# Kernel tuning notes

Hardware: AMD Instinct MI355X
Metric: run time of the kernel (lower is better)

## Reference

```python
import jax, jax.numpy as jnp
import numpy as np

B, T, D = 2, 2048, 1024
H, RANK = 16, 32
DH = D // H  # 64


def setup_inputs() -> dict:
    key = jax.random.key(0)
    ks = jax.random.split(key, 6)
    sd = 1.0 / np.sqrt(D)
    sdh = 1.0 / np.sqrt(DH)
    return {
        "x": jax.random.normal(ks[0], (B, T, D), dtype=jnp.float32),
        "W_qkv": jax.random.normal(ks[1], (D, 3 * D), dtype=jnp.float32) * sd,
        "W_q_lsr": jax.random.normal(ks[2], (H, DH, RANK), dtype=jnp.float32) * sdh,
        "W_k_lsr": jax.random.normal(ks[3], (H, DH, RANK), dtype=jnp.float32) * sdh,
        "lsr_core": jnp.ones((H, RANK), dtype=jnp.float32),
        "W_o": jax.random.normal(ks[4], (D, D), dtype=jnp.float32) * sd,
    }


def reference(x, W_qkv, W_q_lsr, W_k_lsr, lsr_core, W_o):
    b, t, d = x.shape
    # Fused QKV projection
    qkv = x @ W_qkv  # (B, T, 3D)
    q, k, v = jnp.split(qkv, 3, axis=-1)
    # (B, H, T, DH)
    q = q.reshape(b, t, H, DH).transpose(0, 2, 1, 3)
    k = k.reshape(b, t, H, DH).transpose(0, 2, 1, 3)
    v = v.reshape(b, t, H, DH).transpose(0, 2, 1, 3)
    # Low-rank bilinear score: q^T Wq diag(core) Wk^T k
    ql = jnp.einsum("bhtd,hdr->bhtr", q, W_q_lsr)  # (B, H, T, R)
    kl = jnp.einsum("bhsd,hdr->bhsr", k, W_k_lsr)  # (B, H, T, R)
    scale = 1.0 / jnp.sqrt(jnp.asarray(RANK, dtype=x.dtype))
    scores = jnp.einsum("bhtr,bhsr->bhts", ql * lsr_core[None, :, None, :], kl) * scale
    # Causal mask
    causal = jnp.tril(jnp.ones((t, t), dtype=bool))
    scores = jnp.where(causal[None, None], scores, jnp.asarray(-jnp.inf, dtype=scores.dtype))
    attn = jax.nn.softmax(scores, axis=-1)
    y = jnp.einsum("bhts,bhsd->bhtd", attn, v)  # (B, H, T, DH)
    y = y.transpose(0, 2, 1, 3).reshape(b, t, d)
    return y @ W_o
```

## Files before the change

### kernel.cpp

```cpp
#include <hip/hip_runtime.h>
#include <hip/hip_bf16.h>

#define B_  2
#define T_  2048
#define D_  1024
#define H_  16
#define DH_ 64
#define R_  32
#define BT_ (B_*T_)
#define BH_ (B_*H_)

typedef unsigned short u16;
typedef unsigned int   u32;
typedef __attribute__((ext_vector_type(8))) short bhalf8;
typedef __attribute__((ext_vector_type(4))) float floatx4;

#define WSB_FLAG  0
#define WSB_XB    256
#define WSB_WCATT (WSB_XB    + 8388608)
#define WSB_QL    (WSB_WCATT + 4194304)
#define WSB_KL    (WSB_QL    + 4194304)
#define WSB_VT    (WSB_KL    + 4194304)
#define WSB_YB    (WSB_VT    + 8388608)
#define WSB_WOT   (WSB_YB    + 8388608)

#define NEG_ -1.0e30f

__device__ __forceinline__ float bfs(u16 s) {
    union { u32 i; float f; } w; w.i = ((u32)s) << 16; return w.f;
}
__device__ __forceinline__ u16 tob(float f) {
    __hip_bfloat16 h = __float2bfloat16(f);
    return *(u16*)&h;
}
__device__ __forceinline__ u32 pack2(float a, float b) {
    return (u32)tob(a) | ((u32)tob(b) << 16);
}
__device__ __forceinline__ void gload16(const u16* g, u16* l) {
    __builtin_amdgcn_global_load_lds(
        (const __attribute__((address_space(1))) void*)g,
        (__attribute__((address_space(3))) void*)l, 16, 0, 0);
}
__device__ __forceinline__ int detect_isbf(const u32* __restrict__ xw, int lane) {
    int hits = 0;
    #pragma unroll
    for (int i = 0; i < 8; ++i) {
        const u32 w = xw[lane + i * 64];
        const u32 h = w & 0xFFFFu;
        const u32 e = (h >> 7) & 0xFFu;
        if (h == 0u || (e >= 100u && e <= 150u)) ++hits;
    }
    #pragma unroll
    for (int off = 32; off; off >>= 1) hits += __shfl_down(hits, off, 64);
    return __shfl(hits, 0, 64) >= 300;
}

__global__ __launch_bounds__(256) void convert_fused(
    const void* __restrict__ x, u16* __restrict__ xb,
    const void* __restrict__ Wqkv, const void* __restrict__ Wo,
    u16* __restrict__ WcatT, u16* __restrict__ WoT)
{
    __shared__ __align__(16) u16 tile[64 * 72];
    const int tid  = threadIdx.x;
    const int lane = tid & 63;
    const int isbf = detect_isbf((const u32*)x, lane);
    const int blk  = blockIdx.x;

    if (blk < 2048) {
        const int e = blk * 256 + tid;
        if (isbf) {
            ((uint4*)xb)[e] = ((const uint4*)x)[e];
        } else {
            float4 a0 = ((const float4*)x)[2*e];
            float4 a1 = ((const float4*)x)[2*e + 1];
            uint4 o;
            o.x = pack2(a0.x, a0.y); o.y = pack2(a0.z, a0.w);
            o.z = pack2(a1.x, a1.y); o.w = pack2(a1.z, a1.w);
            ((uint4*)xb)[e] = o;
        }
        return;
    }

    int t = blk - 2048;
    const void* src; u16* dst; int srcStride, srcColOff, dstRowOff;
    if (t < 256) { src = Wqkv; dst = WcatT; srcStride = 3*D_; srcColOff = 2*D_; dstRowOff = 1024; }
    else { t -= 256; src = Wo; dst = WoT; srcStride = D_; srcColOff = 0; dstRowOff = 0; }
    const int j0 = (t & 15) * 64;
    const int i0 = (t >> 4) * 64;
    #pragma unroll
    for (int p = 0; p < 2; ++p) {
        const int e = tid + p * 256;
        const int r = e >> 3, ch = e & 7;
        if (isbf) {
            uint4 w = *(const uint4*)((const u16*)src + (size_t)(i0 + r) * srcStride + srcColOff + j0 + ch*8);
            *(uint4*)&tile[r * 72 + ch*8] = w;
        } else {
            const float* s = (const float*)src + (size_t)(i0 + r) * srcStride + srcColOff + j0 + ch*8;
            float4 a0 = *(const float4*)s;
            float4 a1 = *(const float4*)(s + 4);
            uint4 o;
            o.x = pack2(a0.x, a0.y); o.y = pack2(a0.z, a0.w);
            o.z = pack2(a1.x, a1.y); o.w = pack2(a1.z, a1.w);
            *(uint4*)&tile[r * 72 + ch*8] = o;
        }
    }
    __syncthreads();
    #pragma unroll
    for (int p = 0; p < 2; ++p) {
        const int e = tid + p * 256;
        const int c = e >> 3, ch = e & 7;
        u16 tmp[8];
        #pragma unroll
        for (int j = 0; j < 8; ++j) tmp[j] = tile[(ch*8 + j) * 72 + c];
        *(uint4*)(dst + (size_t)(dstRowOff + j0 + c) * D_ + i0 + ch*8) = *(uint4*)tmp;
    }
}

__global__ __launch_bounds__(256) void fold_mfma(
    const void* __restrict__ Wqkv, const void* __restrict__ Wq_lsr,
    const void* __restrict__ Wk_lsr, const void* __restrict__ core,
    u16* __restrict__ WcatT, const void* __restrict__ x)
{
    __shared__ __align__(16) u16 Bq[128 * 72];
    __shared__ __align__(16) u16 Bk[128 * 72];
    __shared__ __align__(16) u16 Aq[32 * 72];
    __shared__ __align__(16) u16 Ak[32 * 72];
    const int tid  = threadIdx.x;
    const int lane = tid & 63;
    const int isbf = detect_isbf((const u32*)x, lane);
    const int w    = tid >> 6;
    const int n16  = lane & 15;
    const int q4   = lane >> 4;
    const int h    = blockIdx.y;
    const int d0   = blockIdx.x * 128;

    #pragma unroll
    for (int p = 0; p < 8; ++p) {
        const int e  = tid + p * 256;
        const int r  = e & 31, dh = e >> 5;
        float aq, ak;
        if (isbf) {
            aq = bfs(((const u16*)Wq_lsr)[(h*DH_ + dh)*R_ + r]);
            ak = bfs(((const u16*)Wk_lsr)[(h*DH_ + dh)*R_ + r]);
        } else {
            aq = ((const float*)Wq_lsr)[(h*DH_ + dh)*R_ + r];
            ak = ((const float*)Wk_lsr)[(h*DH_ + dh)*R_ + r];
        }
        Aq[r * 72 + dh] = tob(aq);
        Ak[r * 72 + dh] = tob(ak);
    }
    #pragma unroll
    for (int p = 0; p < 8; ++p) {
        const int e  = tid + p * 256;
        const int n  = e >> 4, ch = e & 15;
        if (isbf) {
            uint2 wq = *(const uint2*)((const u16*)Wqkv + (size_t)(d0+n)*(3*D_) + h*DH_ + ch*4);
            uint2 wk = *(const uint2*)((const u16*)Wqkv + (size_t)(d0+n)*(3*D_) + D_ + h*DH_ + ch*4);
            *(uint2*)&Bq[n * 72 + ch*4] = wq;
            *(uint2*)&Bk[n * 72 + ch*4] = wk;
        } else {
            float4 fq = *(const float4*)((const float*)Wqkv + (size_t)(d0+n)*(3*D_) + h*DH_ + ch*4);
            float4 fk = *(const float4*)((const float*)Wqkv + (size_t)(d0+n)*(3*D_) + D_ + h*DH_ + ch*4);
            uint2 oq, ok;
            oq.x = pack2(fq.x, fq.y); oq.y = pack2(fq.z, fq.w);
            ok.x = pack2(fk.x, fk.y); ok.y = pack2(fk.z, fk.w);
            *(uint2*)&Bq[n * 72 + ch*4] = oq;
            *(uint2*)&Bk[n * 72 + ch*4] = ok;
        }
    }
    __syncthreads();

    floatx4 accq[2][2], acck[2][2];
    #pragma unroll
    for (int mi = 0; mi < 2; ++mi)
        #pragma unroll
        for (int ni = 0; ni < 2; ++ni) { accq[mi][ni] = (floatx4)(0.f); acck[mi][ni] = (floatx4)(0.f); }

    #pragma unroll
    for (int kk = 0; kk < 2; ++kk) {
        bhalf8 aqf[2], akf[2], bqf[2], bkf[2];
        #pragma unroll
        for (int mi = 0; mi < 2; ++mi) {
            aqf[mi] = *(const bhalf8*)&Aq[(mi*16 + n16) * 72 + kk*32 + q4*8];
            akf[mi] = *(const bhalf8*)&Ak[(mi*16 + n16) * 72 + kk*32 + q4*8];
        }
        #pragma unroll
        for (int ni = 0; ni < 2; ++ni) {
            bqf[ni] = *(const bhalf8*)&Bq[(w*32 + ni*16 + n16) * 72 + kk*32 + q4*8];
            bkf[ni] = *(const bhalf8*)&Bk[(w*32 + ni*16 + n16) * 72 + kk*32 + q4*8];
        }
        #pragma unroll
        for (int mi = 0; mi < 2; ++mi)
            #pragma unroll
            for (int ni = 0; ni < 2; ++ni) {
                accq[mi][ni] = __builtin_amdgcn_mfma_f32_16x16x32_bf16(aqf[mi], bqf[ni], accq[mi][ni], 0, 0, 0);
                acck[mi][ni] = __builtin_amdgcn_mfma_f32_16x16x32_bf16(akf[mi], bkf[ni], acck[mi][ni], 0, 0, 0);
            }
    }

    const float scale = (float)(0.17677669529663687 * 1.4426950408889634);
    #pragma unroll
    for (int mi = 0; mi < 2; ++mi) {
        #pragma unroll
        for (int rr = 0; rr < 4; ++rr) {
            const int r = mi*16 + q4*4 + rr;
            const float cc = (isbf ? bfs(((const u16*)core)[h*R_ + r])
                                   : ((const float*)core)[h*R_ + r]) * scale;
            #pragma unroll
            for (int ni = 0; ni < 2; ++ni) {
                const int d = d0 + w*32 + ni*16 + n16;
                WcatT[(size_t)(h*R_ + r) * D_ + d]       = tob(accq[mi][ni][rr] * cc);
                WcatT[(size_t)(512 + h*R_ + r) * D_ + d] = tob(acck[mi][ni][rr]);
            }
        }
    }
}

__global__ __launch_bounds__(256, 4) void gemm1_mfma(
    const u16* __restrict__ xb, const u16* __restrict__ WcatT,
    u16* __restrict__ ql, u16* __restrict__ kl, u16* __restrict__ v_t)
{
    __shared__ __align__(16) u16 As[128 * 64];
    __shared__ __align__(16) u16 Bs[64 * 64];
    const int tid  = threadIdx.x;
    const int lane = tid & 63;
    const int w    = tid >> 6;
    const int n16  = lane & 15;
    const int q4   = lane >> 4;
    const int wx   = w & 1;
    const int wy   = w >> 1;
    const int bm   = blockIdx.y * 128;
    const int bn   = blockIdx.x * 64;
    const int lrow = lane >> 3;
    const int lcol = (lane & 7) * 8;

    floatx4 acc[4][2];
    #pragma unroll
    for (int i = 0; i < 4; ++i)
        #pragma unroll
        for (int j = 0; j < 2; ++j) acc[i][j] = (floatx4)(0.f);

    for (int kt = 0; kt < D_; kt += 64) {
        #pragma unroll
        for (int i = 0; i < 4; ++i) {
            const int r0 = w*32 + i*8;
            gload16(xb + (size_t)(bm + r0 + lrow) * D_ + kt + lcol, &As[r0 * 64]);
        }
        #pragma unroll
        for (int i = 0; i < 2; ++i) {
            const int r0 = w*16 + i*8;
            gload16(WcatT + (size_t)(bn + r0 + lrow) * D_ + kt + lcol, &Bs[r0 * 64]);
        }
        __syncthreads();
        #pragma unroll
        for (int kk = 0; kk < 2; ++kk) {
            bhalf8 a[4], b[2];
            #pragma unroll
            for (int mi = 0; mi < 4; ++mi)
                a[mi] = *(const bhalf8*)&As[(wy*64 + mi*16 + n16) * 64 + kk*32 + q4*8];
            #pragma unroll
            for (int ni = 0; ni < 2; ++ni)
                b[ni] = *(const bhalf8*)&Bs[(wx*32 + ni*16 + n16) * 64 + kk*32 + q4*8];
            #pragma unroll
            for (int mi = 0; mi < 4; ++mi)
                #pragma unroll
                for (int ni = 0; ni < 2; ++ni)
                    acc[mi][ni] = __builtin_amdgcn_mfma_f32_16x16x32_bf16(
                        a[mi], b[ni], acc[mi][ni], 0, 0, 0);
        }
        __syncthreads();
    }

    if (bn < 1024) {
        #pragma unroll
        for (int mi = 0; mi < 4; ++mi) {
            #pragma unroll
            for (int rr = 0; rr < 4; ++rr) {
                const int row = bm + wy*64 + mi*16 + q4*4 + rr;
                const int b   = row >> 11;
                const int t   = row & (T_ - 1);
                #pragma unroll
                for (int ni = 0; ni < 2; ++ni) {
                    const int col = bn + wx*32 + ni*16 + n16;
                    const u16 val = tob(acc[mi][ni][rr]);
                    if (col < 512) {
                        const int h = col >> 5, r = col & 31;
                        ql[((size_t)(b*H_ + h)*T_ + t)*R_ + r] = val;
                    } else {
                        const int c = col - 512; const int h = c >> 5, r = c & 31;
                        kl[((size_t)(b*H_ + h)*T_ + t)*R_ + r] = val;
                    }
                }
            }
        }
    } else {
        #pragma unroll
        for (int mi = 0; mi < 4; ++mi) {
            const int row0 = bm + wy*64 + mi*16 + q4*4;
            const int b = row0 >> 11;
            const int t = row0 & (T_ - 1);
            #pragma unroll
            for (int ni = 0; ni < 2; ++ni) {
                const int c = bn - 1024 + wx*32 + ni*16 + n16;
                const int h = c >> 6, dh = c & 63;
                uint2 o;
                o.x = pack2(acc[mi][ni][0], acc[mi][ni][1]);
                o.y = pack2(acc[mi][ni][2], acc[mi][ni][3]);
                *(uint2*)(v_t + ((size_t)(b*H_ + h) * DH_ + dh) * T_ + t) = o;
            }
        }
    }
}

__device__ __forceinline__ void softmax_update(
    floatx4 (&Sc)[8], float &mrow, float &lrow, floatx4 (&O)[4], int q4)
{
    float cmax[8];
    #pragma unroll
    for (int c = 0; c < 8; ++c)
        cmax[c] = fmaxf(fmaxf(Sc[c][0], Sc[c][1]), fmaxf(Sc[c][2], Sc[c][3]));
    float rmax = fmaxf(fmaxf(fmaxf(cmax[0], cmax[1]), fmaxf(cmax[2], cmax[3])),
                       fmaxf(fmaxf(cmax[4], cmax[5]), fmaxf(cmax[6], cmax[7])));
    rmax = fmaxf(rmax, __shfl_xor(rmax, 16, 64));
    rmax = fmaxf(rmax, __shfl_xor(rmax, 32, 64));

    const float mn = fmaxf(mrow, rmax);
    const int norescale = __all(rmax <= mrow);

    float csum[8];
    #pragma unroll
    for (int c = 0; c < 8; ++c) {
        #pragma unroll
        for (int r = 0; r < 4; ++r)
            Sc[c][r] = __builtin_amdgcn_exp2f(Sc[c][r] - mn);
        csum[c] = (Sc[c][0] + Sc[c][1]) + (Sc[c][2] + Sc[c][3]);
    }
    float rsum = ((csum[0] + csum[1]) + (csum[2] + csum[3]))
               + ((csum[4] + csum[5]) + (csum[6] + csum[7]));
    rsum += __shfl_xor(rsum, 16, 64);
    rsum += __shfl_xor(rsum, 32, 64);

    if (norescale) {
        lrow += rsum;
    } else {
        const float alpha = __builtin_amdgcn_exp2f(mrow - mn);
        mrow = mn;
        lrow = lrow * alpha + rsum;
        float aO[4];
        #pragma unroll
        for (int r = 0; r < 4; ++r) aO[r] = __shfl(alpha, q4*4 + r, 64);
        #pragma unroll
        for (int c2 = 0; c2 < 4; ++c2)
            #pragma unroll
            for (int r = 0; r < 4; ++r) O[c2][r] *= aO[r];
    }
}

__global__ __launch_bounds__(512, 4) void attn_kernel(
    const u16* __restrict__ ql, const u16* __restrict__ kl,
    const u16* __restrict__ v_t, u16* __restrict__ y)
{
    __shared__ __align__(16) u16 kls[128 * 40];
    __shared__ __align__(16) u16 vsT[64 * 136];

    const int tid  = threadIdx.x;
    const int lane = tid & 63;
    const int w    = tid >> 6;
    const int n16  = lane & 15;
    const int q4   = lane >> 4;
    const int bh   = blockIdx.x;
    const int by   = blockIdx.y;
    const int qt2  = (by < 8) ? (15 - by) : (by - 8);
    const int t0   = qt2 * 128;
    const int nt   = qt2 + 1;

    const u16* qlb = ql + (size_t)bh * T_ * R_;
    const bhalf8 aq = *(const bhalf8*)(qlb + (size_t)(t0 + w*16 + n16) * R_ + q4*8);

    const u16* klb = kl  + (size_t)bh * T_ * R_;
    const u16* vtb = v_t + (size_t)bh * DH_ * T_;
    const int rk = tid >> 2, ck = (tid & 3) * 8;
    const int dv = tid >> 4;
    const int m  = tid & 15;
    const int cv = m * 8;
    const int pb = ((m & 1) << 4) | (((m >> 1) & 1) << 2) | ((m >> 2) << 5);

    uint4 kc0 = *(const uint4*)(klb + (size_t)(rk     ) * R_ + ck);
    uint4 vc0 = *(const uint4*)(vtb + (size_t)(dv     ) * T_ + cv);
    uint4 vc1 = *(const uint4*)(vtb + (size_t)(dv + 32) * T_ + cv);
    uint4 kn0 = kc0, vn0 = vc0, vn1 = vc1;

    float mrow = NEG_, lrow = 0.f;
    floatx4 O[4];
    #pragma unroll
    for (int c = 0; c < 4; ++c) O[c] = (floatx4)(0.f);

    for (int it = 0; it < nt; ++it) {
        const int s0 = it * 128;
        __syncthreads();
        *(uint4*)&kls[rk * 40 + ck] = kc0;
        {
            uint2 t;
            t.x = vc0.x; t.y = vc0.y; *(uint2*)&vsT[(dv     ) * 136 + pb    ] = t;
            t.x = vc0.z; t.y = vc0.w; *(uint2*)&vsT[(dv     ) * 136 + pb + 8] = t;
            t.x = vc1.x; t.y = vc1.y; *(uint2*)&vsT[(dv + 32) * 136 + pb    ] = t;
            t.x = vc1.z; t.y = vc1.w; *(uint2*)&vsT[(dv + 32) * 136 + pb + 8] = t;
        }
        if (it + 1 < nt) {
            const int s1 = s0 + 128;
            kn0 = *(const uint4*)(klb + (size_t)(s1 + rk) * R_ + ck);
            vn0 = *(const uint4*)(vtb + (size_t)(dv     ) * T_ + s1 + cv);
            vn1 = *(const uint4*)(vtb + (size_t)(dv + 32) * T_ + s1 + cv);
        }
        __syncthreads();

        floatx4 Sc[8];
        #pragma unroll
        for (int c = 0; c < 8; ++c) {
            bhalf8 ak = *(const bhalf8*)&kls[(16*c + n16) * 40 + q4*8];
            Sc[c] = __builtin_amdgcn_mfma_f32_16x16x32_bf16(ak, aq, (floatx4)(0.f), 0, 0, 0);
        }

        if (it == nt - 1) {
            const int tq = w*16 + n16;
            #pragma unroll
            for (int c = 0; c < 8; ++c) {
                const int sb = 16*c + 4*q4;
                #pragma unroll
                for (int r = 0; r < 4; ++r)
                    if (sb + r > tq) Sc[c][r] = NEG_;
            }
        }

        softmax_update(Sc, mrow, lrow, O, q4);

        #pragma unroll
        for (int kc = 0; kc < 4; ++kc) {
            union { u32 wd[4]; bhalf8 v; } pu;
            pu.wd[0] = pack2(Sc[2*kc    ][0], Sc[2*kc    ][1]);
            pu.wd[1] = pack2(Sc[2*kc    ][2], Sc[2*kc    ][3]);
            pu.wd[2] = pack2(Sc[2*kc + 1][0], Sc[2*kc + 1][1]);
            pu.wd[3] = pack2(Sc[2*kc + 1][2], Sc[2*kc + 1][3]);
            const bhalf8 pa = pu.v;
            #pragma unroll
            for (int c2 = 0; c2 < 4; ++c2) {
                bhalf8 bv = *(const bhalf8*)&vsT[(16*c2 + n16) * 136 + kc*32 + q4*8];
                O[c2] = __builtin_amdgcn_mfma_f32_16x16x32_bf16(pa, bv, O[c2], 0, 0, 0);
            }
        }

        kc0 = kn0; vc0 = vn0; vc1 = vn1;
    }

    const int b = bh >> 4, h = bh & 15;
    float lb[4];
    #pragma unroll
    for (int r = 0; r < 4; ++r) lb[r] = __shfl(lrow, q4*4 + r, 64);
    #pragma unroll
    for (int r = 0; r < 4; ++r) {
        const float rl = 1.0f / lb[r];
        const int t = t0 + w*16 + q4*4 + r;
        #pragma unroll
        for (int c2 = 0; c2 < 4; ++c2)
            y[((size_t)b * T_ + t) * D_ + h * DH_ + 16*c2 + n16] = tob(O[c2][r] * rl);
    }
}

__global__ __launch_bounds__(256, 4) void out_gemm_mfma(
    const u16* __restrict__ yb, const u16* __restrict__ WoT,
    float* __restrict__ out)
{
    __shared__ __align__(16) u16 As[64 * 64];
    __shared__ __align__(16) u16 Bs[64 * 64];
    const int tid  = threadIdx.x;
    const int lane = tid & 63;
    const int w    = tid >> 6;
    const int n16  = lane & 15;
    const int q4   = lane >> 4;
    const int wx   = w & 1;
    const int wy   = w >> 1;
    const int bm   = blockIdx.y * 64;
    const int bn   = blockIdx.x * 64;
    const int lrow = lane >> 3;
    const int lcol = (lane & 7) * 8;

    floatx4 acc[2][2];
    #pragma unroll
    for (int i = 0; i < 2; ++i)
        #pragma unroll
        for (int j = 0; j < 2; ++j) acc[i][j] = (floatx4)(0.f);

    for (int kt = 0; kt < D_; kt += 64) {
        #pragma unroll
        for (int i = 0; i < 2; ++i) {
            const int r0 = w*16 + i*8;
            gload16(yb  + (size_t)(bm + r0 + lrow) * D_ + kt + lcol, &As[r0 * 64]);
            gload16(WoT + (size_t)(bn + r0 + lrow) * D_ + kt + lcol, &Bs[r0 * 64]);
        }
        __syncthreads();
        #pragma unroll
        for (int kk = 0; kk < 2; ++kk) {
            bhalf8 a[2], b[2];
            #pragma unroll
            for (int mi = 0; mi < 2; ++mi)
                a[mi] = *(const bhalf8*)&As[(wy*32 + mi*16 + n16) * 64 + kk*32 + q4*8];
            #pragma unroll
            for (int ni = 0; ni < 2; ++ni)
                b[ni] = *(const bhalf8*)&Bs[(wx*32 + ni*16 + n16) * 64 + kk*32 + q4*8];
            #pragma unroll
            for (int mi = 0; mi < 2; ++mi)
                #pragma unroll
                for (int ni = 0; ni < 2; ++ni)
                    acc[mi][ni] = __builtin_amdgcn_mfma_f32_16x16x32_bf16(
                        a[mi], b[ni], acc[mi][ni], 0, 0, 0);
        }
        __syncthreads();
    }

    #pragma unroll
    for (int mi = 0; mi < 2; ++mi) {
        #pragma unroll
        for (int rr = 0; rr < 4; ++rr) {
            const int row = bm + wy*32 + mi*16 + q4*4 + rr;
            #pragma unroll
            for (int ni = 0; ni < 2; ++ni) {
                const int col = bn + wx*32 + ni*16 + n16;
                out[(size_t)row * D_ + col] = acc[mi][ni][rr];
            }
        }
    }
}

extern "C" void kernel_launch(void* const* d_in, const int* in_sizes, int n_in,
                              void* d_out, int out_size, void* d_ws, size_t ws_size,
                              hipStream_t stream)
{
    (void)out_size; (void)ws_size;
    const void* in_x = nullptr; const void* in_wqkv = nullptr;
    const void* in_wq = nullptr; const void* in_wk = nullptr;
    const void* in_core = nullptr; const void* in_wo = nullptr;
    for (int i = 0; i < n_in; ++i) {
        const int s = in_sizes[i];
        if      (s == BT_*D_)     { if (!in_x)    in_x    = d_in[i]; }
        else if (s == D_*3*D_)    { if (!in_wqkv) in_wqkv = d_in[i]; }
        else if (s == H_*DH_*R_)  { if (!in_wq)   in_wq   = d_in[i]; else if (!in_wk) in_wk = d_in[i]; }
        else if (s == H_*R_)      { if (!in_core) in_core = d_in[i]; }
        else if (s == D_*D_)      { if (!in_wo)   in_wo   = d_in[i]; }
    }
    if (!in_x)    in_x    = d_in[0];
    if (!in_wqkv) in_wqkv = d_in[1];
    if (!in_wq)   in_wq   = d_in[2];
    if (!in_wk)   in_wk   = d_in[3];
    if (!in_core) in_core = d_in[4];
    if (!in_wo)   in_wo   = d_in[5];

    float* out = (float*)d_out;

    char* ws    = (char*)d_ws;
    u16*  xb    = (u16*)(ws + WSB_XB);
    u16*  WcatT = (u16*)(ws + WSB_WCATT);
    u16*  ql    = (u16*)(ws + WSB_QL);
    u16*  kl    = (u16*)(ws + WSB_KL);
    u16*  v_t   = (u16*)(ws + WSB_VT);
    u16*  yb    = (u16*)(ws + WSB_YB);
    u16*  WoT   = (u16*)(ws + WSB_WOT);

    convert_fused<<<2560, 256, 0, stream>>>(in_x, xb, in_wqkv, in_wo, WcatT, WoT);
    fold_mfma<<<dim3(8, 16), 256, 0, stream>>>(in_wqkv, in_wq, in_wk, in_core, WcatT, in_x);
    gemm1_mfma<<<dim3(32, 32), 256, 0, stream>>>(xb, WcatT, ql, kl, v_t);
    attn_kernel<<<dim3(32, 16), 512, 0, stream>>>(ql, kl, v_t, yb);
    out_gemm_mfma<<<dim3(16, 64), 256, 0, stream>>>(yb, WoT, out);
}
```

Before: 183.0 us.

## Merge prep kernels and restructure attention into per-wave tasks with fragment-layout V

Folds the weight-fold kernel into the conversion kernel so one launch covers all prep work. gemm1 now writes V directly in the MFMA B-fragment order, so the attention kernel can load K and V straight from global memory with no LDS staging and no block barriers. Attention is split into independent per-wave tasks of 16 query rows, ordered longest-first for load balance. The trade-off is more global and L2 traffic, because K/V tiles are no longer shared across the waves of a block, and prefetch overlap is lost.

```diff
diff --git a/kernel.cpp b/kernel.cpp
--- a/kernel.cpp
+++ b/kernel.cpp
@@ -55,16 +55,24 @@
     return __shfl(hits, 0, 64) >= 300;
 }
 
-__global__ __launch_bounds__(256) void convert_fused(
+__global__ __launch_bounds__(256) void prep_kernel(
     const void* __restrict__ x, u16* __restrict__ xb,
     const void* __restrict__ Wqkv, const void* __restrict__ Wo,
+    const void* __restrict__ Wq_lsr, const void* __restrict__ Wk_lsr,
+    const void* __restrict__ core,
     u16* __restrict__ WcatT, u16* __restrict__ WoT)
 {
-    __shared__ __align__(16) u16 tile[64 * 72];
+    __shared__ __align__(16) u16 Bq[128 * 72];
+    __shared__ __align__(16) u16 Bk[128 * 72];
+    __shared__ __align__(16) u16 Aq[32 * 72];
+    __shared__ __align__(16) u16 Ak[32 * 72];
     const int tid  = threadIdx.x;
     const int lane = tid & 63;
     const int isbf = detect_isbf((const u32*)x, lane);
     const int blk  = blockIdx.x;
+    const int w    = tid >> 6;
+    const int n16  = lane & 15;
+    const int q4   = lane >> 4;
 
     if (blk < 2048) {
         const int e = blk * 256 + tid;
@@ -81,58 +89,46 @@
         return;
     }
 
-    int t = blk - 2048;
-    const void* src; u16* dst; int srcStride, srcColOff, dstRowOff;
-    if (t < 256) { src = Wqkv; dst = WcatT; srcStride = 3*D_; srcColOff = 2*D_; dstRowOff = 1024; }
-    else { t -= 256; src = Wo; dst = WoT; srcStride = D_; srcColOff = 0; dstRowOff = 0; }
-    const int j0 = (t & 15) * 64;
-    const int i0 = (t >> 4) * 64;
-    #pragma unroll
-    for (int p = 0; p < 2; ++p) {
-        const int e = tid + p * 256;
-        const int r = e >> 3, ch = e & 7;
-        if (isbf) {
-            uint4 w = *(const uint4*)((const u16*)src + (size_t)(i0 + r) * srcStride + srcColOff + j0 + ch*8);
-            *(uint4*)&tile[r * 72 + ch*8] = w;
-        } else {
-            const float* s = (const float*)src + (size_t)(i0 + r) * srcStride + srcColOff + j0 + ch*8;
-            float4 a0 = *(const float4*)s;
-            float4 a1 = *(const float4*)(s + 4);
-            uint4 o;
-            o.x = pack2(a0.x, a0.y); o.y = pack2(a0.z, a0.w);
-            o.z = pack2(a1.x, a1.y); o.w = pack2(a1.z, a1.w);
-            *(uint4*)&tile[r * 72 + ch*8] = o;
-        }
-    }
-    __syncthreads();
-    #pragma unroll
-    for (int p = 0; p < 2; ++p) {
-        const int e = tid + p * 256;
-        const int c = e >> 3, ch = e & 7;
-        u16 tmp[8];
-        #pragma unroll
-        for (int j = 0; j < 8; ++j) tmp[j] = tile[(ch*8 + j) * 72 + c];
-        *(uint4*)(dst + (size_t)(dstRowOff + j0 + c) * D_ + i0 + ch*8) = *(uint4*)tmp;
-    }
-}
-
-__global__ __launch_bounds__(256) void fold_mfma(
-    const void* __restrict__ Wqkv, const void* __restrict__ Wq_lsr,
-    const void* __restrict__ Wk_lsr, const void* __restrict__ core,
-    u16* __restrict__ WcatT, const void* __restrict__ x)
-{
-    __shared__ __align__(16) u16 Bq[128 * 72];
-    __shared__ __align__(16) u16 Bk[128 * 72];
-    __shared__ __align__(16) u16 Aq[32 * 72];
-    __shared__ __align__(16) u16 Ak[32 * 72];
-    const int tid  = threadIdx.x;
-    const int lane = tid & 63;
-    const int isbf = detect_isbf((const u32*)x, lane);
-    const int w    = tid >> 6;
-    const int n16  = lane & 15;
-    const int q4   = lane >> 4;
-    const int h    = blockIdx.y;
-    const int d0   = blockIdx.x * 128;
+    if (blk < 2560) {
+        int t = blk - 2048;
+        const void* src; u16* dst; int srcStride, srcColOff, dstRowOff;
+        if (t < 256) { src = Wqkv; dst = WcatT; srcStride = 3*D_; srcColOff = 2*D_; dstRowOff = 1024; }
+        else { t -= 256; src = Wo; dst = WoT; srcStride = D_; srcColOff = 0; dstRowOff = 0; }
+        const int j0 = (t & 15) * 64;
+        const int i0 = (t >> 4) * 64;
+        #pragma unroll
+        for (int p = 0; p < 2; ++p) {
+            const int e = tid + p * 256;
+            const int r = e >> 3, ch = e & 7;
+            if (isbf) {
+                uint4 v = *(const uint4*)((const u16*)src + (size_t)(i0 + r) * srcStride + srcColOff + j0 + ch*8);
+                *(uint4*)&Bq[r * 72 + ch*8] = v;
+            } else {
+                const float* s = (const float*)src + (size_t)(i0 + r) * srcStride + srcColOff + j0 + ch*8;
+                float4 a0 = *(const float4*)s;
+                float4 a1 = *(const float4*)(s + 4);
+                uint4 o;
+                o.x = pack2(a0.x, a0.y); o.y = pack2(a0.z, a0.w);
+                o.z = pack2(a1.x, a1.y); o.w = pack2(a1.z, a1.w);
+                *(uint4*)&Bq[r * 72 + ch*8] = o;
+            }
+        }
+        __syncthreads();
+        #pragma unroll
+        for (int p = 0; p < 2; ++p) {
+            const int e = tid + p * 256;
+            const int c = e >> 3, ch = e & 7;
+            u16 tmp[8];
+            #pragma unroll
+            for (int j = 0; j < 8; ++j) tmp[j] = Bq[(ch*8 + j) * 72 + c];
+            *(uint4*)(dst + (size_t)(dstRowOff + j0 + c) * D_ + i0 + ch*8) = *(uint4*)tmp;
+        }
+        return;
+    }
+
+    const int fb = blk - 2560;
+    const int h  = fb & 15;
+    const int d0 = (fb >> 4) * 128;
 
     #pragma unroll
     for (int p = 0; p < 8; ++p) {
@@ -218,7 +214,7 @@
 
 __global__ __launch_bounds__(256, 4) void gemm1_mfma(
     const u16* __restrict__ xb, const u16* __restrict__ WcatT,
-    u16* __restrict__ ql, u16* __restrict__ kl, u16* __restrict__ v_t)
+    u16* __restrict__ ql, u16* __restrict__ kl, u16* __restrict__ vf)
 {
     __shared__ __align__(16) u16 As[128 * 64];
     __shared__ __align__(16) u16 Bs[64 * 64];
@@ -297,16 +293,26 @@
         #pragma unroll
         for (int mi = 0; mi < 4; ++mi) {
             const int row0 = bm + wy*64 + mi*16 + q4*4;
-            const int b = row0 >> 11;
-            const int t = row0 & (T_ - 1);
+            const int b  = row0 >> 11;
+            const int t  = row0 & (T_ - 1);
+            const int tile = t >> 7;
+            const int sl   = t & 127;
+            const int kc   = sl >> 5;
+            const int j2   = (sl >> 4) & 1;
+            const int qv   = (sl >> 2) & 3;
             #pragma unroll
             for (int ni = 0; ni < 2; ++ni) {
-                const int c = bn - 1024 + wx*32 + ni*16 + n16;
-                const int h = c >> 6, dh = c & 63;
+                const int c  = bn - 1024 + wx*32 + ni*16 + n16;
+                const int h  = c >> 6, dh = c & 63;
+                const int bh = b*H_ + h;
+                const int c2 = dh >> 4;
+                const int lv = qv*16 + (dh & 15);
+                u16* dst = vf + ((((size_t)bh*16 + tile)*4 + kc)*4 + c2)*512
+                              + lv*8 + j2*4;
                 uint2 o;
                 o.x = pack2(acc[mi][ni][0], acc[mi][ni][1]);
                 o.y = pack2(acc[mi][ni][2], acc[mi][ni][3]);
-                *(uint2*)(v_t + ((size_t)(b*H_ + h) * DH_ + dh) * T_ + t) = o;
+                *(uint2*)dst = o;
             }
         }
     }
@@ -356,39 +362,25 @@
     }
 }
 
-__global__ __launch_bounds__(512, 4) void attn_kernel(
+__global__ __launch_bounds__(256, 3) void attn_kernel(
     const u16* __restrict__ ql, const u16* __restrict__ kl,
-    const u16* __restrict__ v_t, u16* __restrict__ y)
+    const u16* __restrict__ vf, u16* __restrict__ y)
 {
-    __shared__ __align__(16) u16 kls[128 * 40];
-    __shared__ __align__(16) u16 vsT[64 * 136];
-
     const int tid  = threadIdx.x;
     const int lane = tid & 63;
     const int w    = tid >> 6;
     const int n16  = lane & 15;
     const int q4   = lane >> 4;
-    const int bh   = blockIdx.x;
-    const int by   = blockIdx.y;
-    const int qt2  = (by < 8) ? (15 - by) : (by - 8);
-    const int t0   = qt2 * 128;
-    const int nt   = qt2 + 1;
+    const int task = blockIdx.x * 4 + w;
+    const int qt   = 127 - (task >> 5);
+    const int bh   = task & 31;
+    const int nt   = (qt >> 3) + 1;
 
     const u16* qlb = ql + (size_t)bh * T_ * R_;
-    const bhalf8 aq = *(const bhalf8*)(qlb + (size_t)(t0 + w*16 + n16) * R_ + q4*8);
-
-    const u16* klb = kl  + (size_t)bh * T_ * R_;
-    const u16* vtb = v_t + (size_t)bh * DH_ * T_;
-    const int rk = tid >> 2, ck = (tid & 3) * 8;
-    const int dv = tid >> 4;
-    const int m  = tid & 15;
-    const int cv = m * 8;
-    const int pb = ((m & 1) << 4) | (((m >> 1) & 1) << 2) | ((m >> 2) << 5);
-
-    uint4 kc0 = *(const uint4*)(klb + (size_t)(rk     ) * R_ + ck);
-    uint4 vc0 = *(const uint4*)(vtb + (size_t)(dv     ) * T_ + cv);
-    uint4 vc1 = *(const uint4*)(vtb + (size_t)(dv + 32) * T_ + cv);
-    uint4 kn0 = kc0, vn0 = vc0, vn1 = vc1;
+    const u16* klb = kl + (size_t)bh * T_ * R_;
+    const u16* vfb = vf + (size_t)bh * 131072;
+
+    const bhalf8 aq = *(const bhalf8*)(qlb + (size_t)(16*qt + n16) * R_ + q4*8);
 
     float mrow = NEG_, lrow = 0.f;
     floatx4 O[4];
@@ -396,33 +388,16 @@
     for (int c = 0; c < 4; ++c) O[c] = (floatx4)(0.f);
 
     for (int it = 0; it < nt; ++it) {
-        const int s0 = it * 128;
-        __syncthreads();
-        *(uint4*)&kls[rk * 40 + ck] = kc0;
-        {
-            uint2 t;
-            t.x = vc0.x; t.y = vc0.y; *(uint2*)&vsT[(dv     ) * 136 + pb    ] = t;
-            t.x = vc0.z; t.y = vc0.w; *(uint2*)&vsT[(dv     ) * 136 + pb + 8] = t;
-            t.x = vc1.x; t.y = vc1.y; *(uint2*)&vsT[(dv + 32) * 136 + pb    ] = t;
-            t.x = vc1.z; t.y = vc1.w; *(uint2*)&vsT[(dv + 32) * 136 + pb + 8] = t;
-        }
-        if (it + 1 < nt) {
-            const int s1 = s0 + 128;
-            kn0 = *(const uint4*)(klb + (size_t)(s1 + rk) * R_ + ck);
-            vn0 = *(const uint4*)(vtb + (size_t)(dv     ) * T_ + s1 + cv);
-            vn1 = *(const uint4*)(vtb + (size_t)(dv + 32) * T_ + s1 + cv);
-        }
-        __syncthreads();
-
+        const u16* kt = klb + (size_t)(it*128 + n16) * R_ + q4*8;
         floatx4 Sc[8];
         #pragma unroll
         for (int c = 0; c < 8; ++c) {
-            bhalf8 ak = *(const bhalf8*)&kls[(16*c + n16) * 40 + q4*8];
+            bhalf8 ak = *(const bhalf8*)(kt + (size_t)(16*c) * R_);
             Sc[c] = __builtin_amdgcn_mfma_f32_16x16x32_bf16(ak, aq, (floatx4)(0.f), 0, 0, 0);
         }
 
         if (it == nt - 1) {
-            const int tq = w*16 + n16;
+            const int tq = 16*(qt & 7) + n16;
             #pragma unroll
             for (int c = 0; c < 8; ++c) {
                 const int sb = 16*c + 4*q4;
@@ -434,6 +409,7 @@
 
         softmax_update(Sc, mrow, lrow, O, q4);
 
+        const u16* vt = vfb + (size_t)it * 8192 + lane*8;
         #pragma unroll
         for (int kc = 0; kc < 4; ++kc) {
             union { u32 wd[4]; bhalf8 v; } pu;
@@ -444,12 +420,10 @@
             const bhalf8 pa = pu.v;
             #pragma unroll
             for (int c2 = 0; c2 < 4; ++c2) {
-                bhalf8 bv = *(const bhalf8*)&vsT[(16*c2 + n16) * 136 + kc*32 + q4*8];
+                bhalf8 bv = *(const bhalf8*)(vt + (size_t)(kc*4 + c2) * 512);
                 O[c2] = __builtin_amdgcn_mfma_f32_16x16x32_bf16(pa, bv, O[c2], 0, 0, 0);
             }
         }
-
-        kc0 = kn0; vc0 = vn0; vc1 = vn1;
     }
 
     const int b = bh >> 4, h = bh & 15;
@@ -459,7 +433,7 @@
     #pragma unroll
     for (int r = 0; r < 4; ++r) {
         const float rl = 1.0f / lb[r];
-        const int t = t0 + w*16 + q4*4 + r;
+        const int t = 16*qt + q4*4 + r;
         #pragma unroll
         for (int c2 = 0; c2 < 4; ++c2)
             y[((size_t)b * T_ + t) * D_ + h * DH_ + 16*c2 + n16] = tob(O[c2][r] * rl);
@@ -561,13 +535,13 @@
     u16*  WcatT = (u16*)(ws + WSB_WCATT);
     u16*  ql    = (u16*)(ws + WSB_QL);
     u16*  kl    = (u16*)(ws + WSB_KL);
-    u16*  v_t   = (u16*)(ws + WSB_VT);
+    u16*  vf    = (u16*)(ws + WSB_VT);
     u16*  yb    = (u16*)(ws + WSB_YB);
     u16*  WoT   = (u16*)(ws + WSB_WOT);
 
-    convert_fused<<<2560, 256, 0, stream>>>(in_x, xb, in_wqkv, in_wo, WcatT, WoT);
-    fold_mfma<<<dim3(8, 16), 256, 0, stream>>>(in_wqkv, in_wq, in_wk, in_core, WcatT, in_x);
-    gemm1_mfma<<<dim3(32, 32), 256, 0, stream>>>(xb, WcatT, ql, kl, v_t);
-    attn_kernel<<<dim3(32, 16), 512, 0, stream>>>(ql, kl, v_t, yb);
+    prep_kernel<<<2688, 256, 0, stream>>>(in_x, xb, in_wqkv, in_wo,
+                                          in_wq, in_wk, in_core, WcatT, WoT);
+    gemm1_mfma<<<dim3(32, 32), 256, 0, stream>>>(xb, WcatT, ql, kl, vf);
+    attn_kernel<<<1024, 256, 0, stream>>>(ql, kl, vf, yb);
     out_gemm_mfma<<<dim3(16, 64), 256, 0, stream>>>(yb, WoT, out);
 }
```

Result: no change. 186.5 us (+1.9%).
